# Performance work log

Hardware: AMD Instinct MI355X
Metric: run time of the kernel (lower is better)

The kernel has to match this reference:

```python
import jax, jax.numpy as jnp
import numpy as np

B, NPOS, NNEG, D, NLEM = 8, 512, 512, 128, 32768
MOMENTUM = 0.5
EPS = 1e-12  # F.normalize eps


def setup_inputs() -> dict:
    key = jax.random.key(0)
    k1, k2, k3, k4 = jax.random.split(key, 4)
    x = jax.random.normal(k1, (B, NPOS + NNEG, D), dtype=jnp.float32)
    y = jax.random.randint(k2, (B, NPOS), 0, NPOS).astype(jnp.int64)
    visible = jax.random.randint(k3, (B, NPOS), 0, 2).astype(jnp.int32)
    stdv = 1.0 / np.sqrt(D / 3.0)
    memory = jax.random.uniform(k4, (NLEM, D), dtype=jnp.float32,
                                minval=-stdv, maxval=stdv)
    return {"x": x, "y": y, "visible": visible, "memory": memory, "lru": 3}


def reference(x, y, visible, memory, lru):
    # --- similarity computation (differentiable path) ---
    t = x[:, :NPOS, :]                                  # [B, NPOS, D]
    similarity = jnp.einsum('bpd,md->bpm', t, memory)    # [B, NPOS, NLEM]
    noise_similarity = jnp.einsum('bnd,pd->bnp',
                                  x[:, NPOS:, :], memory[:NPOS])  # [B, NNEG, NPOS]
    y_idx = y.astype(jnp.int64)

    # --- memory bank update (no-grad in original) ---
    vis = visible.astype(x.dtype)[..., None]             # [B, NPOS, 1]
    get = jnp.mean(t * vis, axis=0)                      # [NPOS, D]
    pos_new = memory[:NPOS] * MOMENTUM + get * (1.0 - MOMENTUM)
    neg_flat = x[:, NPOS:, :].reshape(-1, D)             # [B*NNEG, D]
    start = NPOS + lru * NNEG * B                        # lru is a python int
    new_mem = memory.at[start:start + NNEG * B].set(neg_flat)
    new_mem = new_mem.at[:NPOS].set(pos_new)
    norms = jnp.maximum(jnp.linalg.norm(new_mem, axis=1, keepdims=True), EPS)
    new_mem = jax.lax.stop_gradient(new_mem / norms)

    return similarity, y_idx, noise_similarity, new_mem
```

## Files before the change

kernel.cpp:

```cpp
#include <hip/hip_runtime.h>
#include <hip/hip_bf16.h>
#include <cstdint>

#define NPOS 512
#define NNEG 512
#define BATCH 8
#define DDIM 128
#define NLEM 32768
#define NX_ELEM (BATCH * (NPOS + NNEG) * DDIM)
#define NM_ELEM (NLEM * DDIM)

typedef __attribute__((ext_vector_type(4))) float f32x4;
typedef __attribute__((ext_vector_type(16))) float f32x16;
typedef __attribute__((ext_vector_type(8))) short short8;

__device__ __forceinline__ unsigned short f2bf(float f) {
  unsigned u = __float_as_uint(f);
  u = (u + 0x7FFFu + ((u >> 16) & 1u)) >> 16;
  return (unsigned short)u;
}

__device__ __forceinline__ short8 cvt8(f32x4 a0, f32x4 a1) {
  short8 w;
  w[0] = (short)f2bf(a0[0]); w[1] = (short)f2bf(a0[1]);
  w[2] = (short)f2bf(a0[2]); w[3] = (short)f2bf(a0[3]);
  w[4] = (short)f2bf(a1[0]); w[5] = (short)f2bf(a1[1]);
  w[6] = (short)f2bf(a1[2]); w[7] = (short)f2bf(a1[3]);
  return w;
}

__device__ __forceinline__ void async16(const void* g, void* l) {
  __builtin_amdgcn_global_load_lds(
      (const __attribute__((address_space(1))) unsigned int*)g,
      (__attribute__((address_space(3))) unsigned int*)l, 16, 0, 0);
}

__device__ __forceinline__ void newmem_row(int r, int lane, const float* __restrict__ X,
                                           const int* __restrict__ vis,
                                           const float* __restrict__ Mem, int start,
                                           float* __restrict__ out) {
  const int d0 = lane, d1 = lane + 64;
  float v0, v1;
  if (r < NPOS) {
    const float s0 = Mem[(size_t)r * DDIM + d0];
    const float s1 = Mem[(size_t)r * DDIM + d1];
    float a0 = 0.f, a1 = 0.f;
#pragma unroll
    for (int b = 0; b < BATCH; ++b) {
      const float w = (float)vis[b * NPOS + r];
      const float* px = X + (size_t)(b * (NPOS + NNEG) + r) * DDIM;
      a0 += w * px[d0];
      a1 += w * px[d1];
    }
    v0 = 0.5f * s0 + 0.0625f * a0;
    v1 = 0.5f * s1 + 0.0625f * a1;
  } else if (r >= start && r < start + BATCH * NNEG) {
    const int q = r - start;
    const int b = q >> 9, n = q & 511;
    const float* px = X + (size_t)(b * (NPOS + NNEG) + NPOS + n) * DDIM;
    v0 = px[d0];
    v1 = px[d1];
  } else {
    v0 = Mem[(size_t)r * DDIM + d0];
    v1 = Mem[(size_t)r * DDIM + d1];
  }
  float s = v0 * v0 + v1 * v1;
#pragma unroll
  for (int off = 32; off; off >>= 1) s += __shfl_xor(s, off, 64);
  const float inv = 1.0f / fmaxf(sqrtf(s), 1e-12f);
  out[(size_t)r * DDIM + d0] = v0 * inv;
  out[(size_t)r * DDIM + d1] = v1 * inv;
}

__global__ __launch_bounds__(256) void prep_kernel(
    const float* __restrict__ X, const int* __restrict__ y,
    const int* __restrict__ vis, const float* __restrict__ Mem,
    const int* __restrict__ lru_p, unsigned short* __restrict__ xb,
    unsigned short* __restrict__ mb, float* __restrict__ out_y,
    float* __restrict__ out_mem) {
  const int blk = blockIdx.x;
  if (blk < 512) {
    const size_t i = ((size_t)blk * 256 + threadIdx.x) * 8;
    *(short8*)(xb + i) = cvt8(*(const f32x4*)(X + i), *(const f32x4*)(X + i + 4));
  } else if (blk < 2560) {
    const size_t i = ((size_t)(blk - 512) * 256 + threadIdx.x) * 8;
    *(short8*)(mb + i) = cvt8(*(const f32x4*)(Mem + i), *(const f32x4*)(Mem + i + 4));
  } else if (blk < 2576) {
    const int i = (blk - 2560) * 256 + threadIdx.x;
    out_y[i] = (float)y[i];
  } else {
    const int r = (blk - 2576) * 4 + (threadIdx.x >> 6);
    const int start = NPOS + lru_p[0] * (NNEG * BATCH);
    newmem_row(r, threadIdx.x & 63, X, vis, Mem, start, out_mem);
  }
}

__device__ __forceinline__ void hoist_b(const short* Btile, short8 bfr[8][2],
                                        int wc, int la, int lb) {
#pragma unroll
  for (int kk = 0; kk < 8; ++kk)
#pragma unroll
    for (int n2 = 0; n2 < 2; ++n2) {
      const int row = wc * 64 + n2 * 32 + la;
      const int ss = ((kk * 2 + lb) ^ (row & 15)) * 8;
      bfr[kk][n2] = *(const short8*)&Btile[row * 128 + ss];
    }
}

__device__ __forceinline__ void tile_mfma(const short* Atile, const short8 bfr[8][2],
                                          f32x16 acc[2][2], int wr, int la, int lb) {
#pragma unroll
  for (int kk = 0; kk < 8; ++kk) {
    short8 af[2];
#pragma unroll
    for (int m2 = 0; m2 < 2; ++m2) {
      const int row = wr * 64 + m2 * 32 + la;
      const int ss = ((kk * 2 + lb) ^ (row & 15)) * 8;
      af[m2] = *(const short8*)&Atile[row * 128 + ss];
    }
#pragma unroll
    for (int m2 = 0; m2 < 2; ++m2)
#pragma unroll
      for (int n2 = 0; n2 < 2; ++n2)
        acc[m2][n2] = __builtin_amdgcn_mfma_f32_32x32x16_bf16(
            af[m2], bfr[kk][n2], acc[m2][n2], 0, 0, 0);
  }
}

__device__ __forceinline__ void store_acc(const f32x16 acc[2][2],
                                          float* __restrict__ C, int ldc, int m0,
                                          int n0c, int wr, int wc, int la, int lb) {
#pragma unroll
  for (int m2 = 0; m2 < 2; ++m2)
#pragma unroll
    for (int n2 = 0; n2 < 2; ++n2) {
      const int col = n0c + wc * 64 + n2 * 32 + la;
      const int rbase = m0 + wr * 64 + m2 * 32 + lb * 4;
#pragma unroll
      for (int r = 0; r < 16; ++r) {
        const int row = rbase + (r & 3) + 8 * (r >> 2);
        C[(size_t)row * ldc + col] = acc[m2][n2][r];
      }
    }
}

__global__ __launch_bounds__(256, 2) void gemm_band2_kernel(
    const unsigned short* __restrict__ Xb, const unsigned short* __restrict__ Mb,
    float* __restrict__ Csim, float* __restrict__ Cnoise) {
  __shared__ short ldsA[2][128 * 128];

  const int t = threadIdx.x;
  const int lane = t & 63, wv = t >> 6;
  const int rl = lane >> 4, slot = lane & 15;
  const int wr = wv >> 1, wc = wv & 1;
  const int la = lane & 31, lb = lane >> 5;
  const int blk = blockIdx.x;
  const int band = blk >> 1, h = blk & 1;
  const int n0 = band * 128;

  auto stage_tile = [&](short* dst, const unsigned short* src, int rowbase) {
#pragma unroll
    for (int i = 0; i < 8; ++i) {
      const int rowb = wv * 32 + i * 4;
      const int row = rowb + rl;
      const int ss = slot ^ (row & 15);
      async16(src + (size_t)(rowbase + row) * DDIM + ss * 8, &dst[rowb * 128]);
    }
  };

  stage_tile(ldsA[1], Mb, n0);
  {
    const int K0 = h * 16;
    stage_tile(ldsA[0], Xb, (K0 >> 2) * 1024 + (K0 & 3) * 128);
  }
  asm volatile("s_waitcnt vmcnt(0)" ::: "memory");
  __builtin_amdgcn_s_barrier();
  __builtin_amdgcn_sched_barrier(0);

  short8 bfr[8][2];
  hoist_b(ldsA[1], bfr, wc, la, lb);
  asm volatile("s_waitcnt lgkmcnt(0)" ::: "memory");
  __builtin_amdgcn_s_barrier();
  __builtin_amdgcn_sched_barrier(0);

  int p = 0;
  for (int k = 0; k < 16; ++k) {
    if (k + 1 < 16) {
      const int K = h * 16 + k + 1;
      stage_tile(ldsA[p ^ 1], Xb, (K >> 2) * 1024 + (K & 3) * 128);
    }

    f32x16 acc[2][2] = {};
    tile_mfma(ldsA[p], bfr, acc, wr, la, lb);
    store_acc(acc, Csim, NLEM, (h * 16 + k) * 128, n0, wr, wc, la, lb);

    asm volatile("s_waitcnt vmcnt(60)" ::: "memory");
    __builtin_amdgcn_s_barrier();
    __builtin_amdgcn_sched_barrier(0);
    p ^= 1;
  }

  if (blk < 128) {
    const int rp = blk >> 2, cb = blk & 3;
    stage_tile(ldsA[p ^ 1], Xb, (rp >> 2) * 1024 + 512 + (rp & 3) * 128);
    stage_tile(ldsA[p], Mb, cb * 128);
    asm volatile("s_waitcnt vmcnt(0)" ::: "memory");
    __builtin_amdgcn_s_barrier();
    __builtin_amdgcn_sched_barrier(0);
    short8 bfr2[8][2];
    hoist_b(ldsA[p], bfr2, wc, la, lb);
    f32x16 acc[2][2] = {};
    tile_mfma(ldsA[p ^ 1], bfr2, acc, wr, la, lb);
    store_acc(acc, Cnoise, NPOS, rp * 128, cb * 128, wr, wc, la, lb);
  }
}

__global__ __launch_bounds__(256) void gemm_conv_kernel(
    const float* __restrict__ X, const float* __restrict__ Bm,
    float* __restrict__ C, int ldc, int a_off) {
  __shared__ short lds[2 * 128 * 128];
  short* ldsA = lds;
  short* ldsB = lds + 128 * 128;
  const int t = threadIdx.x;
  const int m0 = blockIdx.x * 128;
  const int n0 = blockIdx.y * 128;
  const int slot = t & 15;
  const int rsub = t >> 4;
#pragma unroll
  for (int it = 0; it < 8; ++it) {
    const int row = it * 16 + rsub;
    const int gr = m0 + row;
    const int xrow = ((gr >> 9) << 10) + (gr & 511) + a_off;
    const f32x4* pa = (const f32x4*)(X + (size_t)xrow * DDIM + slot * 8);
    const f32x4* pb = (const f32x4*)(Bm + (size_t)(n0 + row) * DDIM + slot * 8);
    short8 wa = cvt8(pa[0], pa[1]);
    short8 wb = cvt8(pb[0], pb[1]);
    const int ss = (slot ^ (row & 15)) * 8;
    *(short8*)&ldsA[row * 128 + ss] = wa;
    *(short8*)&ldsB[row * 128 + ss] = wb;
  }
  __syncthreads();
  const int lane = t & 63;
  const int wv = t >> 6;
  const int wr = wv >> 1, wc = wv & 1;
  const int la = lane & 31, lb = lane >> 5;
  short8 bfr[8][2];
  hoist_b(ldsB, bfr, wc, la, lb);
  f32x16 acc[2][2] = {};
  tile_mfma(ldsA, bfr, acc, wr, la, lb);
  store_acc(acc, C, ldc, m0, n0, wr, wc, la, lb);
}

__global__ void y_kernel(const int* __restrict__ y, float* __restrict__ out) {
  const int i = blockIdx.x * blockDim.x + threadIdx.x;
  if (i < BATCH * NPOS) out[i] = (float)y[i];
}

__global__ __launch_bounds__(256) void newmem_kernel(
    const float* __restrict__ X, const int* __restrict__ vis,
    const float* __restrict__ Mem, const int* __restrict__ lru_p,
    float* __restrict__ out) {
  const int r = blockIdx.x * 4 + (threadIdx.x >> 6);
  const int start = NPOS + lru_p[0] * (NNEG * BATCH);
  newmem_row(r, threadIdx.x & 63, X, vis, Mem, start, out);
}

extern "C" void kernel_launch(void* const* d_in, const int* in_sizes, int n_in,
                              void* d_out, int out_size, void* d_ws, size_t ws_size,
                              hipStream_t stream) {
  const float* x = (const float*)d_in[0];
  const int* y = (const int*)d_in[1];
  const int* visible = (const int*)d_in[2];
  const float* memory = (const float*)d_in[3];
  const int* lru = (const int*)d_in[4];
  float* out = (float*)d_out;

  const size_t OFF_Y = (size_t)BATCH * NPOS * NLEM;
  const size_t OFF_NOISE = OFF_Y + (size_t)BATCH * NPOS;
  const size_t OFF_MEM = OFF_NOISE + (size_t)BATCH * NNEG * NPOS;

  const size_t need = (size_t)(NX_ELEM + NM_ELEM) * 2;
  if (ws_size >= need) {
    unsigned short* xb = (unsigned short*)d_ws;
    unsigned short* mb = xb + NX_ELEM;
    prep_kernel<<<10768, 256, 0, stream>>>(
        x, y, visible, memory, lru, xb, mb, out + OFF_Y, out + OFF_MEM);
    gemm_band2_kernel<<<512, 256, 0, stream>>>(xb, mb, out, out + OFF_NOISE);
  } else {
    gemm_conv_kernel<<<dim3(32, 256), 256, 0, stream>>>(x, memory, out, NLEM, 0);
    gemm_conv_kernel<<<dim3(32, 4), 256, 0, stream>>>(x, memory, out + OFF_NOISE, NPOS, NPOS);
    y_kernel<<<16, 256, 0, stream>>>(y, out + OFF_Y);
    newmem_kernel<<<NLEM / 4, 256, 0, stream>>>(x, visible, memory, lru, out + OFF_MEM);
  }
}
```

Before: 121.1 us.

## Fuse memory bf16 conversion and bulk row normalization into GEMM kernel

```diff
diff --git a/kernel.cpp b/kernel.cpp
--- a/kernel.cpp
+++ b/kernel.cpp
@@ -8,7 +8,6 @@
 #define DDIM 128
 #define NLEM 32768
 #define NX_ELEM (BATCH * (NPOS + NNEG) * DDIM)
-#define NM_ELEM (NLEM * DDIM)
 
 typedef __attribute__((ext_vector_type(4))) float f32x4;
 typedef __attribute__((ext_vector_type(16))) float f32x16;
@@ -76,22 +75,18 @@
     const float* __restrict__ X, const int* __restrict__ y,
     const int* __restrict__ vis, const float* __restrict__ Mem,
     const int* __restrict__ lru_p, unsigned short* __restrict__ xb,
-    unsigned short* __restrict__ mb, float* __restrict__ out_y,
-    float* __restrict__ out_mem) {
+    float* __restrict__ out_y, float* __restrict__ out_mem) {
   const int blk = blockIdx.x;
   if (blk < 512) {
     const size_t i = ((size_t)blk * 256 + threadIdx.x) * 8;
     *(short8*)(xb + i) = cvt8(*(const f32x4*)(X + i), *(const f32x4*)(X + i + 4));
-  } else if (blk < 2560) {
-    const size_t i = ((size_t)(blk - 512) * 256 + threadIdx.x) * 8;
-    *(short8*)(mb + i) = cvt8(*(const f32x4*)(Mem + i), *(const f32x4*)(Mem + i + 4));
-  } else if (blk < 2576) {
-    const int i = (blk - 2560) * 256 + threadIdx.x;
-    out_y[i] = (float)y[i];
-  } else {
-    const int r = (blk - 2576) * 4 + (threadIdx.x >> 6);
+  } else if (blk < 640) {
+    const int r = (blk - 512) * 4 + (threadIdx.x >> 6);
     const int start = NPOS + lru_p[0] * (NNEG * BATCH);
     newmem_row(r, threadIdx.x & 63, X, vis, Mem, start, out_mem);
+  } else {
+    const int i = (blk - 640) * 256 + threadIdx.x;
+    out_y[i] = (float)y[i];
   }
 }
 
@@ -144,9 +139,26 @@
     }
 }
 
+__device__ __forceinline__ void convert_b_tile(const float* __restrict__ Mem,
+                                               int rbase, short* dst, int t) {
+  const int srow = t >> 1, scol = (t & 1) * 64, sslot0 = scol >> 3;
+  f32x4 vb[16];
+  const f32x4* pb = (const f32x4*)(Mem + (size_t)(rbase + srow) * DDIM + scol);
+#pragma unroll
+  for (int j = 0; j < 16; ++j) vb[j] = pb[j];
+#pragma unroll
+  for (int j = 0; j < 8; ++j) {
+    short8 w = cvt8(vb[2 * j], vb[2 * j + 1]);
+    const int ss = (sslot0 + j) ^ (srow & 15);
+    *(short8*)&dst[srow * 128 + ss * 8] = w;
+  }
+}
+
 __global__ __launch_bounds__(256, 2) void gemm_band2_kernel(
-    const unsigned short* __restrict__ Xb, const unsigned short* __restrict__ Mb,
-    float* __restrict__ Csim, float* __restrict__ Cnoise) {
+    const unsigned short* __restrict__ Xb, const float* __restrict__ Mem,
+    const float* __restrict__ X, const int* __restrict__ lru_p,
+    float* __restrict__ Csim, float* __restrict__ Cnoise,
+    float* __restrict__ out_mem) {
   __shared__ short ldsA[2][128 * 128];
 
   const int t = threadIdx.x;
@@ -157,6 +169,7 @@
   const int blk = blockIdx.x;
   const int band = blk >> 1, h = blk & 1;
   const int n0 = band * 128;
+  const int nm_start = NPOS + lru_p[0] * (NNEG * BATCH);
 
   auto stage_tile = [&](short* dst, const unsigned short* src, int rowbase) {
 #pragma unroll
@@ -168,12 +181,12 @@
     }
   };
 
-  stage_tile(ldsA[1], Mb, n0);
   {
     const int K0 = h * 16;
     stage_tile(ldsA[0], Xb, (K0 >> 2) * 1024 + (K0 & 3) * 128);
   }
-  asm volatile("s_waitcnt vmcnt(0)" ::: "memory");
+  convert_b_tile(Mem, n0, ldsA[1], t);
+  asm volatile("s_waitcnt vmcnt(0) lgkmcnt(0)" ::: "memory");
   __builtin_amdgcn_s_barrier();
   __builtin_amdgcn_sched_barrier(0);
 
@@ -190,9 +203,34 @@
       stage_tile(ldsA[p ^ 1], Xb, (K >> 2) * 1024 + (K & 3) * 128);
     }
 
+    const int s_idx = k * 4 + wv;
+    const int r = 512 + s_idx * 512 + blk;
+    float v0 = 0.f, v1 = 0.f;
+    const bool do_nm = (s_idx < 63);
+    if (do_nm) {
+      const float* src;
+      if (r >= nm_start && r < nm_start + BATCH * NNEG) {
+        const int q = r - nm_start;
+        src = X + (size_t)((q >> 9) * (NPOS + NNEG) + NPOS + (q & 511)) * DDIM;
+      } else {
+        src = Mem + (size_t)r * DDIM;
+      }
+      v0 = src[lane];
+      v1 = src[lane + 64];
+    }
+
     f32x16 acc[2][2] = {};
     tile_mfma(ldsA[p], bfr, acc, wr, la, lb);
     store_acc(acc, Csim, NLEM, (h * 16 + k) * 128, n0, wr, wc, la, lb);
+
+    if (do_nm) {
+      float s = v0 * v0 + v1 * v1;
+#pragma unroll
+      for (int off = 32; off; off >>= 1) s += __shfl_xor(s, off, 64);
+      const float inv = 1.0f / fmaxf(sqrtf(s), 1e-12f);
+      out_mem[(size_t)r * DDIM + lane] = v0 * inv;
+      out_mem[(size_t)r * DDIM + lane + 64] = v1 * inv;
+    }
 
     asm volatile("s_waitcnt vmcnt(60)" ::: "memory");
     __builtin_amdgcn_s_barrier();
@@ -202,15 +240,15 @@
 
   if (blk < 128) {
     const int rp = blk >> 2, cb = blk & 3;
-    stage_tile(ldsA[p ^ 1], Xb, (rp >> 2) * 1024 + 512 + (rp & 3) * 128);
-    stage_tile(ldsA[p], Mb, cb * 128);
-    asm volatile("s_waitcnt vmcnt(0)" ::: "memory");
+    stage_tile(ldsA[1], Xb, (rp >> 2) * 1024 + 512 + (rp & 3) * 128);
+    convert_b_tile(Mem, cb * 128, ldsA[0], t);
+    asm volatile("s_waitcnt vmcnt(0) lgkmcnt(0)" ::: "memory");
     __builtin_amdgcn_s_barrier();
     __builtin_amdgcn_sched_barrier(0);
     short8 bfr2[8][2];
-    hoist_b(ldsA[p], bfr2, wc, la, lb);
+    hoist_b(ldsA[0], bfr2, wc, la, lb);
     f32x16 acc[2][2] = {};
-    tile_mfma(ldsA[p ^ 1], bfr2, acc, wr, la, lb);
+    tile_mfma(ldsA[1], bfr2, acc, wr, la, lb);
     store_acc(acc, Cnoise, NPOS, rp * 128, cb * 128, wr, wc, la, lb);
   }
 }
@@ -279,13 +317,13 @@
   const size_t OFF_NOISE = OFF_Y + (size_t)BATCH * NPOS;
   const size_t OFF_MEM = OFF_NOISE + (size_t)BATCH * NNEG * NPOS;
 
-  const size_t need = (size_t)(NX_ELEM + NM_ELEM) * 2;
+  const size_t need = (size_t)NX_ELEM * 2;
   if (ws_size >= need) {
     unsigned short* xb = (unsigned short*)d_ws;
-    unsigned short* mb = xb + NX_ELEM;
-    prep_kernel<<<10768, 256, 0, stream>>>(
-        x, y, visible, memory, lru, xb, mb, out + OFF_Y, out + OFF_MEM);
-    gemm_band2_kernel<<<512, 256, 0, stream>>>(xb, mb, out, out + OFF_NOISE);
+    prep_kernel<<<656, 256, 0, stream>>>(x, y, visible, memory, lru, xb,
+                                         out + OFF_Y, out + OFF_MEM);
+    gemm_band2_kernel<<<512, 256, 0, stream>>>(xb, memory, x, lru, out,
+                                               out + OFF_NOISE, out + OFF_MEM);
   } else {
     gemm_conv_kernel<<<dim3(32, 256), 256, 0, stream>>>(x, memory, out, NLEM, 0);
     gemm_conv_kernel<<<dim3(32, 4), 256, 0, stream>>>(x, memory, out + OFF_NOISE, NPOS, NPOS);
```

Result: slower. 129.2 us (+6.7%).

## Move new-memory normalization for non-positive rows into GEMM kernel tail

Applied to the files above, without the earlier changes.

```diff
diff --git a/kernel.cpp b/kernel.cpp
--- a/kernel.cpp
+++ b/kernel.cpp
@@ -146,7 +146,9 @@
 
 __global__ __launch_bounds__(256, 2) void gemm_band2_kernel(
     const unsigned short* __restrict__ Xb, const unsigned short* __restrict__ Mb,
-    float* __restrict__ Csim, float* __restrict__ Cnoise) {
+    const float* __restrict__ X, const float* __restrict__ Mem,
+    const int* __restrict__ lru_p, float* __restrict__ Csim,
+    float* __restrict__ Cnoise, float* __restrict__ out_mem) {
   __shared__ short ldsA[2][128 * 128];
 
   const int t = threadIdx.x;
@@ -213,6 +215,48 @@
     tile_mfma(ldsA[p ^ 1], bfr2, acc, wr, la, lb);
     store_acc(acc, Cnoise, NPOS, rp * 128, cb * 128, wr, wc, la, lb);
   }
+
+  {
+    const int nm_start = NPOS + lru_p[0] * (NNEG * BATCH);
+    auto row_ptr = [&](int idx) -> const float* {
+      const int r = 512 + idx * 512 + blk;
+      if (r >= nm_start && r < nm_start + BATCH * NNEG) {
+        const int q = r - nm_start;
+        return X + (size_t)((q >> 9) * (NPOS + NNEG) + NPOS + (q & 511)) * DDIM;
+      }
+      return Mem + (size_t)r * DDIM;
+    };
+
+    int idx = wv;
+    float c0 = 0.f, c1 = 0.f;
+    {
+      const float* pr = row_ptr(idx);
+      c0 = pr[lane];
+      c1 = pr[lane + 64];
+    }
+#pragma unroll 1
+    for (int i = 0; i < 16; ++i) {
+      const int nidx = idx + 4;
+      float q0 = 0.f, q1 = 0.f;
+      if (i + 1 < 16 && nidx < 63) {
+        const float* pr = row_ptr(nidx);
+        q0 = pr[lane];
+        q1 = pr[lane + 64];
+      }
+      if (idx < 63) {
+        const int r = 512 + idx * 512 + blk;
+        float s = c0 * c0 + c1 * c1;
+#pragma unroll
+        for (int off = 32; off; off >>= 1) s += __shfl_xor(s, off, 64);
+        const float inv = 1.0f / fmaxf(sqrtf(s), 1e-12f);
+        out_mem[(size_t)r * DDIM + lane] = c0 * inv;
+        out_mem[(size_t)r * DDIM + lane + 64] = c1 * inv;
+      }
+      c0 = q0;
+      c1 = q1;
+      idx = nidx;
+    }
+  }
 }
 
 __global__ __launch_bounds__(256) void gemm_conv_kernel(
@@ -283,9 +327,10 @@
   if (ws_size >= need) {
     unsigned short* xb = (unsigned short*)d_ws;
     unsigned short* mb = xb + NX_ELEM;
-    prep_kernel<<<10768, 256, 0, stream>>>(
+    prep_kernel<<<2704, 256, 0, stream>>>(
         x, y, visible, memory, lru, xb, mb, out + OFF_Y, out + OFF_MEM);
-    gemm_band2_kernel<<<512, 256, 0, stream>>>(xb, mb, out, out + OFF_NOISE);
+    gemm_band2_kernel<<<512, 256, 0, stream>>>(xb, mb, x, memory, lru, out,
+                                               out + OFF_NOISE, out + OFF_MEM);
   } else {
     gemm_conv_kernel<<<dim3(32, 256), 256, 0, stream>>>(x, memory, out, NLEM, 0);
     gemm_conv_kernel<<<dim3(32, 4), 256, 0, stream>>>(x, memory, out + OFF_NOISE, NPOS, NPOS);
```

Result: slower. 140.6 us (+16.1%).
